# Optimization experiments

Hardware: AMD Instinct MI355X
Metric: run time of the kernel (lower is better)

The kernel has to match this reference:

```python
import jax, jax.numpy as jnp
import numpy as np

N_HEAD = 8
PREFIX_LEN = 77  # hardcoded text prefix length in the 'prefix' model_type branch
MASKED_BIAS = -10000.0


def setup_inputs() -> dict:
    key = jax.random.key(0)
    k1, k2, k3 = jax.random.split(key, 3)
    B, S, D = 8, 1024, 1024
    x = jax.random.normal(k1, (B, S, D), dtype=jnp.float32)
    attention_mask = jnp.zeros((B, 1, 1, S), dtype=jnp.float32)
    W_attn = jax.random.normal(k2, (D, 3 * D), dtype=jnp.float32) * 0.02
    b_attn = jnp.zeros((3 * D,), dtype=jnp.float32)
    W_proj = jax.random.normal(k3, (D, D), dtype=jnp.float32) * 0.02
    b_proj = jnp.zeros((D,), dtype=jnp.float32)
    return {"x": x, "attention_mask": attention_mask, "W_attn": W_attn,
            "b_attn": b_attn, "W_proj": W_proj, "b_proj": b_proj}


def _prefix_mask(S):
    # Rows < 77: attend only to cols < 77 (bidirectional prefix).
    # Rows >= 77: standard causal (cols <= row).
    row = jnp.arange(S)[:, None]
    col = jnp.arange(S)[None, :]
    return jnp.where(row < PREFIX_LEN, col < PREFIX_LEN, col <= row)  # [S, S] bool


def reference(x, attention_mask, W_attn, b_attn, W_proj, b_proj):
    B, S, D = x.shape
    H = N_HEAD
    hd = D // H
    qkv = x @ W_attn + b_attn                         # [B, S, 3D]
    q, k, v = jnp.split(qkv, 3, axis=-1)
    q = q.reshape(B, S, H, hd).transpose(0, 2, 1, 3)  # [B, H, S, hd]
    k = k.reshape(B, S, H, hd).transpose(0, 2, 1, 3)
    v = v.reshape(B, S, H, hd).transpose(0, 2, 1, 3)
    w = jnp.einsum('bhqd,bhkd->bhqk', q, k) / jnp.sqrt(jnp.float32(hd))
    mask = _prefix_mask(S)[None, None]                # [1, 1, S, S]
    w = jnp.where(mask, w, jnp.float32(MASKED_BIAS))
    w = w + attention_mask                            # additive mask [B,1,1,S]
    w = jax.nn.softmax(w, axis=-1)
    # dropout omitted (eval-mode reference)
    a = jnp.einsum('bhqk,bhkd->bhqd', w, v)           # [B, H, S, hd]
    a = a.transpose(0, 2, 1, 3).reshape(B, S, D)      # merge heads
    return a @ W_proj + b_proj
```

## Files before the change

kernel.cpp:

```cpp
#include <hip/hip_runtime.h>
#include <cstdint>
#include <cstddef>

#define B_  8
#define S_  1024
#define D_  1024
#define H_  8
#define HD_ 128
#define N3_ 3072
#define PREFIX 77
#define MASKED_BIAS -10000.0f

typedef __bf16 bf16x8 __attribute__((ext_vector_type(8)));
typedef float  f32x4  __attribute__((ext_vector_type(4)));

__device__ __forceinline__ unsigned short f2bf_rne(float f) {
    unsigned int u = __float_as_uint(f);
    u += 0x7FFFu + ((u >> 16) & 1u);
    return (unsigned short)(u >> 16);
}
__device__ __forceinline__ float bf2f(unsigned short h) {
    return __uint_as_float(((unsigned int)h) << 16);
}

__device__ __forceinline__ void load_lds16(const unsigned short* g, unsigned short* l) {
    __builtin_amdgcn_global_load_lds(
        (const __attribute__((address_space(1))) unsigned int*)g,
        (__attribute__((address_space(3))) unsigned int*)l,
        16, 0, 0);
}

__global__ void prep(const float* __restrict__ x, unsigned short* __restrict__ xb,
                     const float* __restrict__ Wa, unsigned short* __restrict__ wta,
                     const float* __restrict__ Wp, unsigned short* __restrict__ wph) {
    __shared__ float tile[32][33];
    const int bid = (int)blockIdx.x;
    const int tid = threadIdx.x;
    if (bid < 8192) {
        const int i = bid * 256 + tid;
        float4 v = reinterpret_cast<const float4*>(x)[i];
        ushort4 o;
        o.x = f2bf_rne(v.x); o.y = f2bf_rne(v.y); o.z = f2bf_rne(v.z); o.w = f2bf_rne(v.w);
        reinterpret_cast<ushort4*>(xb)[i] = o;
        return;
    }
    const float* in; unsigned short* out; int C, bx, by;
    if (bid < 8192 + 3072) {
        const int lb = bid - 8192;
        in = Wa; out = wta; C = N3_;
        bx = lb % 96; by = lb / 96;
    } else {
        const int lb = bid - 11264;
        in = Wp; out = wph; C = D_;
        bx = lb & 31; by = lb >> 5;
    }
    const int c0 = bx * 32, r0 = by * 32;
    const int tx = tid & 31, ty = tid >> 5;
    #pragma unroll
    for (int i = 0; i < 4; ++i)
        tile[ty + i * 8][tx] = in[(size_t)(r0 + ty + i * 8) * C + c0 + tx];
    __syncthreads();
    #pragma unroll
    for (int i = 0; i < 4; ++i)
        out[(size_t)(c0 + ty + i * 8) * D_ + r0 + tx] = f2bf_rne(tile[tx][ty + i * 8]);
}

__global__ void transpose_v(const unsigned short* __restrict__ v, unsigned short* __restrict__ vt) {
    __shared__ unsigned short tile[32][33];
    const int bh = blockIdx.z;
    const int d0 = blockIdx.x * 32, s0 = blockIdx.y * 32;
    const unsigned short* vi = v + (size_t)bh * S_ * HD_;
    unsigned short* vo = vt + (size_t)bh * S_ * HD_;
    const int tx = threadIdx.x, ty = threadIdx.y;
    #pragma unroll
    for (int i = 0; i < 4; ++i)
        tile[ty + i * 8][tx] = vi[(size_t)(s0 + ty + i * 8) * HD_ + d0 + tx];
    __syncthreads();
    #pragma unroll
    for (int i = 0; i < 4; ++i)
        vo[(size_t)(d0 + ty + i * 8) * S_ + s0 + tx] = tile[tx][ty + i * 8];
}

__global__ __launch_bounds__(256) void gemm_qkv(
    const unsigned short* __restrict__ xb,
    const unsigned short* __restrict__ wt,
    const float* __restrict__ bias,
    unsigned short* __restrict__ qb,
    unsigned short* __restrict__ kb,
    unsigned short* __restrict__ vb) {
    __shared__ unsigned short As[2][128 * 32];
    __shared__ unsigned short Bs[2][128 * 32];
    const int tid = threadIdx.x;
    const int bid = (int)blockIdx.x;
    const int xcd = bid & 7, l = bid >> 3;
    const int m0 = (xcd * 8 + (l & 7)) * 128;
    const int n0 = (l >> 3) * 128;
    const int w = tid >> 6, lane = tid & 63;
    const int wm = (w >> 1) * 64, wn = (w & 1) * 64;
    const int l15 = lane & 15, l4 = lane >> 4;
    const int srow = lane >> 2;
    const int sg = ((lane & 3) ^ ((lane >> 3) & 3)) * 8;
    const unsigned short* gA0 = xb + (size_t)(m0 + w * 32 + srow) * 1024 + sg;
    const unsigned short* gA1 = gA0 + 16 * 1024;
    const unsigned short* gB0 = wt + (size_t)(n0 + w * 32 + srow) * 1024 + sg;
    const unsigned short* gB1 = gB0 + 16 * 1024;
    const int ch8 = (l4 ^ ((l15 >> 1) & 3)) * 8;
    int aoff[4], boff[4];
    #pragma unroll
    for (int i = 0; i < 4; ++i) {
        aoff[i] = (wm + i * 16 + l15) * 32 + ch8;
        boff[i] = (wn + i * 16 + l15) * 32 + ch8;
    }
    f32x4 acc[4][4] = {};
    auto stage = [&](int kt, int bi) {
        const int k0 = kt * 32;
        load_lds16(gA0 + k0, &As[bi][w * 1024]);
        load_lds16(gA1 + k0, &As[bi][w * 1024 + 512]);
        load_lds16(gB0 + k0, &Bs[bi][w * 1024]);
        load_lds16(gB1 + k0, &Bs[bi][w * 1024 + 512]);
    };
    stage(0, 0);
    asm volatile("s_waitcnt vmcnt(0)" ::: "memory");
    __syncthreads();
    for (int kt = 0; kt < 32; ++kt) {
        const int cur = kt & 1;
        if (kt < 31) stage(kt + 1, cur ^ 1);
        bf16x8 af[4], bfr[4];
        #pragma unroll
        for (int i = 0; i < 4; ++i) {
            af[i]  = *(const bf16x8*)&As[cur][aoff[i]];
            bfr[i] = *(const bf16x8*)&Bs[cur][boff[i]];
        }
        #pragma unroll
        for (int mi = 0; mi < 4; ++mi)
            #pragma unroll
            for (int ni = 0; ni < 4; ++ni)
                acc[mi][ni] = __builtin_amdgcn_mfma_f32_16x16x32_bf16(af[mi], bfr[ni], acc[mi][ni], 0, 0, 0);
        if (kt < 31) {
            asm volatile("s_waitcnt vmcnt(0)" ::: "memory");
            __syncthreads();
        }
    }
    #pragma unroll
    for (int mi = 0; mi < 4; ++mi) {
        #pragma unroll
        for (int ni = 0; ni < 4; ++ni) {
            const int col = n0 + wn + ni * 16 + l15;
            const float bv = bias[col];
            const int part = col >> 10;
            const int cidx = col & 1023;
            const int h = cidx >> 7, d = cidx & 127;
            unsigned short* dst = (part == 0) ? qb : ((part == 1) ? kb : vb);
            #pragma unroll
            for (int r = 0; r < 4; ++r) {
                const int row = m0 + wm + mi * 16 + l4 * 4 + r;
                const int b = row >> 10, s = row & 1023;
                dst[((size_t)(b * 8 + h) * 1024 + s) * 128 + d] = f2bf_rne(acc[mi][ni][r] + bv);
            }
        }
    }
}

__global__ __launch_bounds__(256, 2) void attn(
    const unsigned short* __restrict__ qb,
    const unsigned short* __restrict__ kb,
    const unsigned short* __restrict__ vt,
    const float* __restrict__ amask,
    unsigned short* __restrict__ ah,
    unsigned short* __restrict__ al) {
    __shared__ unsigned short Ks[2][64 * 128];
    __shared__ unsigned short Vs[128 * 64];
    __shared__ unsigned short P_lds[4][16 * 72];
    const int tid = threadIdx.x;
    const int w = tid >> 6, lane = tid & 63;
    const int l15 = lane & 15, l4 = lane >> 4;
    const int bidx = (int)blockIdx.x;
    const int qt = 15 - (bidx >> 6);
    const int h = bidx & 7, b = (bidx >> 3) & 7;
    const int bh = b * H_ + h;
    const unsigned short* Q = qb + (size_t)bh * S_ * HD_;
    const unsigned short* Kg = kb + (size_t)bh * S_ * HD_;
    const unsigned short* Vg = vt + (size_t)bh * S_ * HD_;
    unsigned short* pl = P_lds[w];
    const float L2E = 1.44269504088896341f;
    const float SCL = 0.08838834764831845f * L2E;
    const float M2  = 8.0f;

    const int q0 = qt * 64;
    const int q0w = q0 + w * 16;
    bf16x8 qf[4];
    #pragma unroll
    for (int s = 0; s < 4; ++s)
        qf[s] = *(const bf16x8*)(Q + (size_t)(q0w + l15) * 128 + s * 32 + l4 * 8);
    float lsum[4] = {0.f, 0.f, 0.f, 0.f};
    f32x4 o[8] = {};
    const int limit = (q0 + 64 > PREFIX) ? (q0 + 64) : PREFIX;
    const int nkt = (limit + 63) >> 6;

    const int kr = lane >> 4;
    const int kc = lane & 15;
    const int vr = lane >> 3;
    const int vc = lane & 7;

    #pragma unroll
    for (int j = 0; j < 4; ++j) {
        const int rl = w * 16 + j * 4 + kr;
        const int g = kc ^ (j * 4 + kr);
        load_lds16(Kg + (size_t)rl * 128 + g * 8, &Ks[0][(w * 16 + j * 4) * 128]);
    }

    for (int kt = 0; kt < nkt; ++kt) {
        const int kbase = kt * 64;
        const int cur = kt & 1;
        __syncthreads();
        if (kt + 1 < nkt) {
            const int kb2 = (kt + 1) * 64;
            #pragma unroll
            for (int j = 0; j < 4; ++j) {
                const int rl = w * 16 + j * 4 + kr;
                const int g = kc ^ (j * 4 + kr);
                load_lds16(Kg + (size_t)(kb2 + rl) * 128 + g * 8, &Ks[cur ^ 1][(w * 16 + j * 4) * 128]);
            }
        }
        #pragma unroll
        for (int j = 0; j < 4; ++j) {
            const int rv = w * 32 + j * 8 + vr;
            const int g = vc ^ vr;
            load_lds16(Vg + (size_t)rv * 1024 + kbase + g * 8, &Vs[(w * 32 + j * 8) * 64]);
        }
        const bool full = (kbase + 64 <= PREFIX) || (q0w >= PREFIX && kbase + 64 <= q0w);
        #pragma unroll
        for (int t = 0; t < 4; ++t) {
            f32x4 sa = {};
            #pragma unroll
            for (int s = 0; s < 4; ++s) {
                bf16x8 kf = *(const bf16x8*)&Ks[cur][(t * 16 + l15) * 128 + (((s * 4 + l4) ^ l15) * 8)];
                sa = __builtin_amdgcn_mfma_f32_16x16x32_bf16(qf[s], kf, sa, 0, 0, 0);
            }
            const int kcol = kbase + t * 16 + l15;
            const float am = fmaf(amask[b * S_ + kcol], L2E, -M2);
            float p[4];
            if (full) {
                #pragma unroll
                for (int r = 0; r < 4; ++r) p[r] = exp2f(fmaf(sa[r], SCL, am));
            } else {
                #pragma unroll
                for (int r = 0; r < 4; ++r) {
                    const int row = q0w + l4 * 4 + r;
                    const bool keep = (row < PREFIX) ? (kcol < PREFIX) : (kcol <= row);
                    const float e = exp2f(fmaf(sa[r], SCL, am));
                    p[r] = keep ? e : 0.f;
                }
            }
            #pragma unroll
            for (int r = 0; r < 4; ++r) {
                lsum[r] += p[r];
                pl[(l4 * 4 + r) * 72 + t * 16 + l15] = f2bf_rne(p[r]);
            }
        }
        bf16x8 pf0 = *(const bf16x8*)&pl[l15 * 72 + l4 * 8];
        bf16x8 pf1 = *(const bf16x8*)&pl[l15 * 72 + 32 + l4 * 8];
        __syncthreads();
        #pragma unroll
        for (int n = 0; n < 8; ++n) {
            bf16x8 vf = *(const bf16x8*)&Vs[(n * 16 + l15) * 64 + ((l4 ^ (l15 & 7)) * 8)];
            o[n] = __builtin_amdgcn_mfma_f32_16x16x32_bf16(pf0, vf, o[n], 0, 0, 0);
        }
        #pragma unroll
        for (int n = 0; n < 8; ++n) {
            bf16x8 vf = *(const bf16x8*)&Vs[(n * 16 + l15) * 64 + ((((4 + l4) ^ (l15 & 7))) * 8)];
            o[n] = __builtin_amdgcn_mfma_f32_16x16x32_bf16(pf1, vf, o[n], 0, 0, 0);
        }
    }
    float inv_l[4];
    #pragma unroll
    for (int r = 0; r < 4; ++r) {
        float sm = lsum[r];
        sm += __shfl_xor(sm, 1);
        sm += __shfl_xor(sm, 2);
        sm += __shfl_xor(sm, 4);
        sm += __shfl_xor(sm, 8);
        inv_l[r] = 1.0f / sm;
    }
    #pragma unroll
    for (int n = 0; n < 8; ++n) {
        const int d = n * 16 + l15;
        #pragma unroll
        for (int r = 0; r < 4; ++r) {
            const int s = q0w + l4 * 4 + r;
            const float val = o[n][r] * inv_l[r];
            const size_t idx = ((size_t)b * 1024 + s) * 1024 + h * 128 + d;
            unsigned short hv = f2bf_rne(val);
            ah[idx] = hv;
            al[idx] = f2bf_rne(val - bf2f(hv));
        }
    }
}

__global__ __launch_bounds__(256) void gemm_proj(
    const unsigned short* __restrict__ ahp,
    const unsigned short* __restrict__ alp,
    const unsigned short* __restrict__ wh,
    const float* __restrict__ bias,
    float* __restrict__ out) {
    __shared__ unsigned short As[2][128 * 32];
    __shared__ unsigned short Bs[2][128 * 32];
    const int tid = threadIdx.x;
    const int bid = (int)blockIdx.x;
    const int xcd = bid & 7, l = bid >> 3;
    const int m0 = (xcd * 8 + (l >> 3)) * 128;
    const int n0 = (l & 7) * 128;
    const int w = tid >> 6, lane = tid & 63;
    const int wm = (w >> 1) * 64, wn = (w & 1) * 64;
    const int l15 = lane & 15, l4 = lane >> 4;
    const int srow = lane >> 2;
    const int sg = ((lane & 3) ^ ((lane >> 3) & 3)) * 8;
    const size_t offA = (size_t)(m0 + w * 32 + srow) * 1024 + sg;
    const size_t offB = (size_t)(n0 + w * 32 + srow) * 1024 + sg;
    const int ch8 = (l4 ^ ((l15 >> 1) & 3)) * 8;
    int aoff[4], boff[4];
    #pragma unroll
    for (int i = 0; i < 4; ++i) {
        aoff[i] = (wm + i * 16 + l15) * 32 + ch8;
        boff[i] = (wn + i * 16 + l15) * 32 + ch8;
    }
    f32x4 acc[4][4] = {};
    auto stage = [&](int tt, int bi) {
        const int k0 = (tt & 31) * 32;
        const unsigned short* Ap = ((tt >> 5) ? alp : ahp) + offA + k0;
        const unsigned short* Bp = wh + offB + k0;
        load_lds16(Ap, &As[bi][w * 1024]);
        load_lds16(Ap + 16 * 1024, &As[bi][w * 1024 + 512]);
        load_lds16(Bp, &Bs[bi][w * 1024]);
        load_lds16(Bp + 16 * 1024, &Bs[bi][w * 1024 + 512]);
    };
    stage(0, 0);
    asm volatile("s_waitcnt vmcnt(0)" ::: "memory");
    __syncthreads();
    for (int kt = 0; kt < 64; ++kt) {
        const int cur = kt & 1;
        if (kt < 63) stage(kt + 1, cur ^ 1);
        bf16x8 af[4], bfr[4];
        #pragma unroll
        for (int i = 0; i < 4; ++i) {
            af[i]  = *(const bf16x8*)&As[cur][aoff[i]];
            bfr[i] = *(const bf16x8*)&Bs[cur][boff[i]];
        }
        #pragma unroll
        for (int mi = 0; mi < 4; ++mi)
            #pragma unroll
            for (int ni = 0; ni < 4; ++ni)
                acc[mi][ni] = __builtin_amdgcn_mfma_f32_16x16x32_bf16(af[mi], bfr[ni], acc[mi][ni], 0, 0, 0);
        if (kt < 63) {
            asm volatile("s_waitcnt vmcnt(0)" ::: "memory");
            __syncthreads();
        }
    }
    #pragma unroll
    for (int mi = 0; mi < 4; ++mi) {
        #pragma unroll
        for (int ni = 0; ni < 4; ++ni) {
            const int col = n0 + wn + ni * 16 + l15;
            const float bv = bias[col];
            #pragma unroll
            for (int r = 0; r < 4; ++r) {
                const int row = m0 + wm + mi * 16 + l4 * 4 + r;
                out[(size_t)row * 1024 + col] = acc[mi][ni][r] + bv;
            }
        }
    }
}

extern "C" void kernel_launch(void* const* d_in, const int* in_sizes, int n_in,
                              void* d_out, int out_size, void* d_ws, size_t ws_size,
                              hipStream_t stream) {
    const float* x      = (const float*)d_in[0];
    const float* amask  = (const float*)d_in[1];
    const float* W_attn = (const float*)d_in[2];
    const float* b_attn = (const float*)d_in[3];
    const float* W_proj = (const float*)d_in[4];
    const float* b_proj = (const float*)d_in[5];
    float* out = (float*)d_out;

    char* ws = (char*)d_ws;
    unsigned short* xb  = (unsigned short*)(ws);
    unsigned short* wta = (unsigned short*)(ws + 16777216);
    unsigned short* qb  = (unsigned short*)(ws + 23068672);
    unsigned short* kb2 = (unsigned short*)(ws + 39845888);
    unsigned short* vb  = (unsigned short*)(ws + 56623104);
    unsigned short* vtb = (unsigned short*)(ws + 73400320);
    unsigned short* ahi = (unsigned short*)(ws + 90177536);
    unsigned short* alo = (unsigned short*)(ws + 106954752);
    unsigned short* wph = (unsigned short*)(ws + 123731968);

    prep<<<dim3(12288), 256, 0, stream>>>(x, xb, W_attn, wta, W_proj, wph);
    gemm_qkv<<<dim3(1536), 256, 0, stream>>>(xb, wta, b_attn, qb, kb2, vb);
    transpose_v<<<dim3(HD_ / 32, S_ / 32, B_ * H_), dim3(32, 8), 0, stream>>>(vb, vtb);
    attn<<<dim3(1024), 256, 0, stream>>>(qb, kb2, vtb, amask, ahi, alo);
    gemm_proj<<<dim3(512), 256, 0, stream>>>(ahi, alo, wph, b_proj, out);
}
```

Before: 277.1 us.

## Triple-buffer GEMM K-loops and fuse V transpose into QKV epilogue

After: 281.8 us. Within noise of the previous version (+1.7%).

```diff
diff --git a/kernel.cpp b/kernel.cpp
--- a/kernel.cpp
+++ b/kernel.cpp
@@ -65,31 +65,15 @@
         out[(size_t)(c0 + ty + i * 8) * D_ + r0 + tx] = f2bf_rne(tile[tx][ty + i * 8]);
 }
 
-__global__ void transpose_v(const unsigned short* __restrict__ v, unsigned short* __restrict__ vt) {
-    __shared__ unsigned short tile[32][33];
-    const int bh = blockIdx.z;
-    const int d0 = blockIdx.x * 32, s0 = blockIdx.y * 32;
-    const unsigned short* vi = v + (size_t)bh * S_ * HD_;
-    unsigned short* vo = vt + (size_t)bh * S_ * HD_;
-    const int tx = threadIdx.x, ty = threadIdx.y;
-    #pragma unroll
-    for (int i = 0; i < 4; ++i)
-        tile[ty + i * 8][tx] = vi[(size_t)(s0 + ty + i * 8) * HD_ + d0 + tx];
-    __syncthreads();
-    #pragma unroll
-    for (int i = 0; i < 4; ++i)
-        vo[(size_t)(d0 + ty + i * 8) * S_ + s0 + tx] = tile[tx][ty + i * 8];
-}
-
 __global__ __launch_bounds__(256) void gemm_qkv(
     const unsigned short* __restrict__ xb,
     const unsigned short* __restrict__ wt,
     const float* __restrict__ bias,
     unsigned short* __restrict__ qb,
     unsigned short* __restrict__ kb,
-    unsigned short* __restrict__ vb) {
-    __shared__ unsigned short As[2][128 * 32];
-    __shared__ unsigned short Bs[2][128 * 32];
+    unsigned short* __restrict__ vtb) {
+    __shared__ unsigned short As[3][128 * 32];
+    __shared__ unsigned short Bs[3][128 * 32];
     const int tid = threadIdx.x;
     const int bid = (int)blockIdx.x;
     const int xcd = bid & 7, l = bid >> 3;
@@ -105,42 +89,49 @@
     const unsigned short* gB0 = wt + (size_t)(n0 + w * 32 + srow) * 1024 + sg;
     const unsigned short* gB1 = gB0 + 16 * 1024;
     const int ch8 = (l4 ^ ((l15 >> 1) & 3)) * 8;
-    int aoff[4], boff[4];
-    #pragma unroll
-    for (int i = 0; i < 4; ++i) {
-        aoff[i] = (wm + i * 16 + l15) * 32 + ch8;
-        boff[i] = (wn + i * 16 + l15) * 32 + ch8;
-    }
     f32x4 acc[4][4] = {};
-    auto stage = [&](int kt, int bi) {
-        const int k0 = kt * 32;
-        load_lds16(gA0 + k0, &As[bi][w * 1024]);
-        load_lds16(gA1 + k0, &As[bi][w * 1024 + 512]);
-        load_lds16(gB0 + k0, &Bs[bi][w * 1024]);
-        load_lds16(gB1 + k0, &Bs[bi][w * 1024 + 512]);
-    };
-    stage(0, 0);
+
+#define G_STAGE(KT, BUF) do {                                   \
+    const int k0s = (KT) * 32;                                  \
+    load_lds16(gA0 + k0s, &As[BUF][w * 1024]);                  \
+    load_lds16(gA1 + k0s, &As[BUF][w * 1024 + 512]);            \
+    load_lds16(gB0 + k0s, &Bs[BUF][w * 1024]);                  \
+    load_lds16(gB1 + k0s, &Bs[BUF][w * 1024 + 512]);            \
+} while (0)
+
+#define G_COMPUTE(BUF) do {                                     \
+    bf16x8 af[4], bfr[4];                                       \
+    _Pragma("unroll") for (int i = 0; i < 4; ++i) {             \
+        af[i]  = *(const bf16x8*)&As[BUF][(wm + i * 16 + l15) * 32 + ch8]; \
+        bfr[i] = *(const bf16x8*)&Bs[BUF][(wn + i * 16 + l15) * 32 + ch8]; \
+    }                                                           \
+    _Pragma("unroll") for (int mi = 0; mi < 4; ++mi)            \
+        _Pragma("unroll") for (int ni = 0; ni < 4; ++ni)        \
+            acc[mi][ni] = __builtin_amdgcn_mfma_f32_16x16x32_bf16(af[mi], bfr[ni], acc[mi][ni], 0, 0, 0); \
+} while (0)
+
+#define SYNC_CNT4() do {                                        \
+    asm volatile("s_waitcnt vmcnt(4)" ::: "memory");            \
+    __builtin_amdgcn_s_barrier();                               \
+    __builtin_amdgcn_sched_barrier(0);                          \
+} while (0)
+
+    G_STAGE(0, 0);
+    G_STAGE(1, 1);
+    asm volatile("s_waitcnt vmcnt(4)" ::: "memory");
+    __builtin_amdgcn_s_barrier();
+    __builtin_amdgcn_sched_barrier(0);
+    for (int tb = 0; tb < 30; tb += 3) {
+        G_STAGE(tb + 2, 2); G_COMPUTE(0); SYNC_CNT4();
+        G_STAGE(tb + 3, 0); G_COMPUTE(1); SYNC_CNT4();
+        G_STAGE(tb + 4, 1); G_COMPUTE(2); SYNC_CNT4();
+    }
+    G_COMPUTE(0);
     asm volatile("s_waitcnt vmcnt(0)" ::: "memory");
-    __syncthreads();
-    for (int kt = 0; kt < 32; ++kt) {
-        const int cur = kt & 1;
-        if (kt < 31) stage(kt + 1, cur ^ 1);
-        bf16x8 af[4], bfr[4];
-        #pragma unroll
-        for (int i = 0; i < 4; ++i) {
-            af[i]  = *(const bf16x8*)&As[cur][aoff[i]];
-            bfr[i] = *(const bf16x8*)&Bs[cur][boff[i]];
-        }
-        #pragma unroll
-        for (int mi = 0; mi < 4; ++mi)
-            #pragma unroll
-            for (int ni = 0; ni < 4; ++ni)
-                acc[mi][ni] = __builtin_amdgcn_mfma_f32_16x16x32_bf16(af[mi], bfr[ni], acc[mi][ni], 0, 0, 0);
-        if (kt < 31) {
-            asm volatile("s_waitcnt vmcnt(0)" ::: "memory");
-            __syncthreads();
-        }
-    }
+    __builtin_amdgcn_s_barrier();
+    __builtin_amdgcn_sched_barrier(0);
+    G_COMPUTE(1);
+
     #pragma unroll
     for (int mi = 0; mi < 4; ++mi) {
         #pragma unroll
@@ -150,12 +141,20 @@
             const int part = col >> 10;
             const int cidx = col & 1023;
             const int h = cidx >> 7, d = cidx & 127;
-            unsigned short* dst = (part == 0) ? qb : ((part == 1) ? kb : vb);
-            #pragma unroll
-            for (int r = 0; r < 4; ++r) {
-                const int row = m0 + wm + mi * 16 + l4 * 4 + r;
-                const int b = row >> 10, s = row & 1023;
-                dst[((size_t)(b * 8 + h) * 1024 + s) * 128 + d] = f2bf_rne(acc[mi][ni][r] + bv);
+            const int row0 = m0 + wm + mi * 16 + l4 * 4;
+            const int b = row0 >> 10, s0r = row0 & 1023;
+            if (part == 2) {
+                ushort4 vv;
+                vv.x = f2bf_rne(acc[mi][ni][0] + bv);
+                vv.y = f2bf_rne(acc[mi][ni][1] + bv);
+                vv.z = f2bf_rne(acc[mi][ni][2] + bv);
+                vv.w = f2bf_rne(acc[mi][ni][3] + bv);
+                *(ushort4*)&vtb[((size_t)(b * 8 + h) * 128 + d) * 1024 + s0r] = vv;
+            } else {
+                unsigned short* dst = part ? kb : qb;
+                #pragma unroll
+                for (int r = 0; r < 4; ++r)
+                    dst[((size_t)(b * 8 + h) * 1024 + (s0r + r)) * 128 + d] = f2bf_rne(acc[mi][ni][r] + bv);
             }
         }
     }
@@ -303,8 +302,8 @@
     const unsigned short* __restrict__ wh,
     const float* __restrict__ bias,
     float* __restrict__ out) {
-    __shared__ unsigned short As[2][128 * 32];
-    __shared__ unsigned short Bs[2][128 * 32];
+    __shared__ unsigned short As[3][128 * 32];
+    __shared__ unsigned short Bs[3][128 * 32];
     const int tid = threadIdx.x;
     const int bid = (int)blockIdx.x;
     const int xcd = bid & 7, l = bid >> 3;
@@ -316,46 +315,41 @@
     const int srow = lane >> 2;
     const int sg = ((lane & 3) ^ ((lane >> 3) & 3)) * 8;
     const size_t offA = (size_t)(m0 + w * 32 + srow) * 1024 + sg;
-    const size_t offB = (size_t)(n0 + w * 32 + srow) * 1024 + sg;
+    const unsigned short* gAh = ahp + offA;
+    const unsigned short* gAl = alp + offA;
+    const unsigned short* gB0 = wh + (size_t)(n0 + w * 32 + srow) * 1024 + sg;
+    const unsigned short* gB1 = gB0 + 16 * 1024;
     const int ch8 = (l4 ^ ((l15 >> 1) & 3)) * 8;
-    int aoff[4], boff[4];
-    #pragma unroll
-    for (int i = 0; i < 4; ++i) {
-        aoff[i] = (wm + i * 16 + l15) * 32 + ch8;
-        boff[i] = (wn + i * 16 + l15) * 32 + ch8;
-    }
     f32x4 acc[4][4] = {};
-    auto stage = [&](int tt, int bi) {
-        const int k0 = (tt & 31) * 32;
-        const unsigned short* Ap = ((tt >> 5) ? alp : ahp) + offA + k0;
-        const unsigned short* Bp = wh + offB + k0;
-        load_lds16(Ap, &As[bi][w * 1024]);
-        load_lds16(Ap + 16 * 1024, &As[bi][w * 1024 + 512]);
-        load_lds16(Bp, &Bs[bi][w * 1024]);
-        load_lds16(Bp + 16 * 1024, &Bs[bi][w * 1024 + 512]);
-    };
-    stage(0, 0);
+
+#define P_STAGE(KT, BUF) do {                                   \
+    const int tt = (KT);                                        \
+    const int k0s = (tt & 31) * 32;                             \
+    const unsigned short* Ap = ((tt & 32) ? gAl : gAh) + k0s;   \
+    load_lds16(Ap, &As[BUF][w * 1024]);                         \
+    load_lds16(Ap + 16 * 1024, &As[BUF][w * 1024 + 512]);       \
+    load_lds16(gB0 + k0s, &Bs[BUF][w * 1024]);                  \
+    load_lds16(gB1 + k0s, &Bs[BUF][w * 1024 + 512]);            \
+} while (0)
+
+    P_STAGE(0, 0);
+    P_STAGE(1, 1);
+    asm volatile("s_waitcnt vmcnt(4)" ::: "memory");
+    __builtin_amdgcn_s_barrier();
+    __builtin_amdgcn_sched_barrier(0);
+    for (int tb = 0; tb < 60; tb += 3) {
+        P_STAGE(tb + 2, 2); G_COMPUTE(0); SYNC_CNT4();
+        P_STAGE(tb + 3, 0); G_COMPUTE(1); SYNC_CNT4();
+        P_STAGE(tb + 4, 1); G_COMPUTE(2); SYNC_CNT4();
+    }
+    P_STAGE(62, 2); G_COMPUTE(0); SYNC_CNT4();
+    P_STAGE(63, 0); G_COMPUTE(1); SYNC_CNT4();
+    G_COMPUTE(2);
     asm volatile("s_waitcnt vmcnt(0)" ::: "memory");
-    __syncthreads();
-    for (int kt = 0; kt < 64; ++kt) {
-        const int cur = kt & 1;
-        if (kt < 63) stage(kt + 1, cur ^ 1);
-        bf16x8 af[4], bfr[4];
-        #pragma unroll
-        for (int i = 0; i < 4; ++i) {
-            af[i]  = *(const bf16x8*)&As[cur][aoff[i]];
-            bfr[i] = *(const bf16x8*)&Bs[cur][boff[i]];
-        }
-        #pragma unroll
-        for (int mi = 0; mi < 4; ++mi)
-            #pragma unroll
-            for (int ni = 0; ni < 4; ++ni)
-                acc[mi][ni] = __builtin_amdgcn_mfma_f32_16x16x32_bf16(af[mi], bfr[ni], acc[mi][ni], 0, 0, 0);
-        if (kt < 63) {
-            asm volatile("s_waitcnt vmcnt(0)" ::: "memory");
-            __syncthreads();
-        }
-    }
+    __builtin_amdgcn_s_barrier();
+    __builtin_amdgcn_sched_barrier(0);
+    G_COMPUTE(0);
+
     #pragma unroll
     for (int mi = 0; mi < 4; ++mi) {
         #pragma unroll
@@ -387,15 +381,13 @@
     unsigned short* wta = (unsigned short*)(ws + 16777216);
     unsigned short* qb  = (unsigned short*)(ws + 23068672);
     unsigned short* kb2 = (unsigned short*)(ws + 39845888);
-    unsigned short* vb  = (unsigned short*)(ws + 56623104);
     unsigned short* vtb = (unsigned short*)(ws + 73400320);
     unsigned short* ahi = (unsigned short*)(ws + 90177536);
     unsigned short* alo = (unsigned short*)(ws + 106954752);
     unsigned short* wph = (unsigned short*)(ws + 123731968);
 
     prep<<<dim3(12288), 256, 0, stream>>>(x, xb, W_attn, wta, W_proj, wph);
-    gemm_qkv<<<dim3(1536), 256, 0, stream>>>(xb, wta, b_attn, qb, kb2, vb);
-    transpose_v<<<dim3(HD_ / 32, S_ / 32, B_ * H_), dim3(32, 8), 0, stream>>>(vb, vtb);
+    gemm_qkv<<<dim3(1536), 256, 0, stream>>>(xb, wta, b_attn, qb, kb2, vtb);
     attn<<<dim3(1024), 256, 0, stream>>>(qb, kb2, vtb, amask, ahi, alo);
     gemm_proj<<<dim3(512), 256, 0, stream>>>(ahi, alo, wph, b_proj, out);
 }
```
